# Kernel optimization log

Measured on AMD Instinct MI355X. Metric: run time of the kernel, lower is better.

Reference implementation:

```python
import jax, jax.numpy as jnp
import numpy as np

MAX_PIXELS = 8  # matches init max_pixels; width=256 matches input W


def _shift_one(img, cy, cx, vy, vx):
    # img: [C,H,W]; cy:[H] cx:[W] clamped source indices; vy/vx validity masks
    out = img[:, cy, :][:, :, cx]            # nearest gather == exact integer shift
    mask = (vy[:, None] & vx[None, :]).astype(img.dtype)  # zeros padding
    return out * mask


def setup_inputs() -> dict:
    key = jax.random.key(0)
    k1, k2 = jax.random.split(key)
    N, C, H, W = 128, 3, 256, 256
    inp = jax.random.normal(k1, (N, C, H, W), dtype=jnp.float32)
    # raw shifts in [0, 2*max_pixels]; reference subtracts MAX_PIXELS -> [-8, 8]
    shifts = jax.random.randint(k2, (N, 2), 0, 2 * MAX_PIXELS + 1, dtype=jnp.int32)
    return {"input": inp, "shifts": shifts}


def reference(input, shifts):
    # Equivalent of affine_grid(theta with bias=shift/(W/2)) + grid_sample(nearest,
    # padding_mode='zeros', align_corners=False): out[n,c,i,j] = in[n,c,i+dy,j+dx]
    # with zero padding out of range. shifts[:,0]=dx (x/width), shifts[:,1]=dy.
    N, C, H, W = input.shape
    s = shifts - MAX_PIXELS                       # [N,2] in [-max_pixels, max_pixels]
    j = jnp.arange(W, dtype=jnp.int32)
    i = jnp.arange(H, dtype=jnp.int32)
    src_x = j[None, :] + s[:, 0:1]                # [N,W]
    src_y = i[None, :] + s[:, 1:2]                # [N,H]
    vx = (src_x >= 0) & (src_x < W)
    vy = (src_y >= 0) & (src_y < H)
    cx = jnp.clip(src_x, 0, W - 1)
    cy = jnp.clip(src_y, 0, H - 1)
    return jax.vmap(_shift_one)(input, cy, cx, vy, vx)
```

## Files before the change

kernel.cpp:

```cpp
#include <hip/hip_runtime.h>


#define MAXPIX 8
#define W 256
#define H 256
#define CCH 3

__global__ __launch_bounds__(256) void shift_kernel(
    const float* __restrict__ in,
    const int* __restrict__ shifts,
    float* __restrict__ out,
    int total_rows)
{
    const int lane = threadIdx.x & 63;
    const int wave_in_block = threadIdx.x >> 6;
    const int rows_per_block = 256 / 64;
    int row = blockIdx.x * rows_per_block + wave_in_block;
    const int row_stride = gridDim.x * rows_per_block;

    for (; row < total_rows; row += row_stride) {
        const int i  = row & (H - 1);
        const int nc = row >> 8;
        const int n  = nc / CCH;

        const int sx = shifts[2 * n]     - MAXPIX;
        const int sy = shifts[2 * n + 1] - MAXPIX;

        const int src_y = i + sy;
        float4 v = {0.f, 0.f, 0.f, 0.f};
        if ((unsigned)src_y < (unsigned)H) {
            const float* __restrict__ src =
                in + ((long)nc * H + src_y) * W;
            const int j0 = (lane << 2) + sx;
            v.x = ((unsigned)(j0 + 0) < (unsigned)W) ? src[j0 + 0] : 0.f;
            v.y = ((unsigned)(j0 + 1) < (unsigned)W) ? src[j0 + 1] : 0.f;
            v.z = ((unsigned)(j0 + 2) < (unsigned)W) ? src[j0 + 2] : 0.f;
            v.w = ((unsigned)(j0 + 3) < (unsigned)W) ? src[j0 + 3] : 0.f;
        }
        *reinterpret_cast<float4*>(out + (long)row * W + (lane << 2)) = v;
    }
}

extern "C" void kernel_launch(void* const* d_in, const int* in_sizes, int n_in,
                              void* d_out, int out_size, void* d_ws, size_t ws_size,
                              hipStream_t stream) {
    const float* in     = (const float*)d_in[0];
    const int*   shifts = (const int*)d_in[1];
    float*       out    = (float*)d_out;

    const int total_rows = out_size / W;

    const int rows_per_block = 4;
    int blocks = (total_rows + rows_per_block - 1) / rows_per_block;
    if (blocks > 2048) blocks = 2048;

    shift_kernel<<<dim3(blocks), dim3(256), 0, stream>>>(in, shifts, out, total_rows);
}
```

Baseline: 38.19 us.

## Batch four rows per wave with branchless clamped loads and nontemporal stores

Replaces the grid-stride loop with a fixed mapping where each wave handles four consecutive rows. All loads are issued up front using clamped indices with masking afterwards, so there are no divergent branches and more memory requests are in flight. Output stores use nontemporal hints to avoid polluting cache, the shift index is made wave-uniform via readfirstlane, and the grid is no longer capped at 2048 blocks. The cost is more registers per thread and redundant loads for fully out-of-range rows.

```diff
diff --git a/kernel.cpp b/kernel.cpp
--- a/kernel.cpp
+++ b/kernel.cpp
@@ -6,6 +6,8 @@
 #define H 256
 #define CCH 3
 
+typedef float f32x4 __attribute__((ext_vector_type(4)));
+
 __global__ __launch_bounds__(256) void shift_kernel(
     const float* __restrict__ in,
     const int* __restrict__ shifts,
@@ -13,31 +15,51 @@
     int total_rows)
 {
     const int lane = threadIdx.x & 63;
-    const int wave_in_block = threadIdx.x >> 6;
-    const int rows_per_block = 256 / 64;
-    int row = blockIdx.x * rows_per_block + wave_in_block;
-    const int row_stride = gridDim.x * rows_per_block;
+    const int wid  = threadIdx.x >> 6;
+    constexpr int R = 4;
+    const int row0 = (blockIdx.x * 4 + wid) * R;
+    if (row0 >= total_rows) return;
 
-    for (; row < total_rows; row += row_stride) {
-        const int i  = row & (H - 1);
-        const int nc = row >> 8;
-        const int n  = nc / CCH;
+    f32x4 v[R];
+
+    #pragma unroll
+    for (int r = 0; r < R; ++r) {
+        int rr = row0 + r;
+        rr = min(rr, total_rows - 1);
+        const int i  = rr & (H - 1);
+        const int nc = rr >> 8;
+        int n = nc / CCH;
+        n = __builtin_amdgcn_readfirstlane(n);
 
         const int sx = shifts[2 * n]     - MAXPIX;
         const int sy = shifts[2 * n + 1] - MAXPIX;
 
-        const int src_y = i + sy;
-        float4 v = {0.f, 0.f, 0.f, 0.f};
-        if ((unsigned)src_y < (unsigned)H) {
-            const float* __restrict__ src =
-                in + ((long)nc * H + src_y) * W;
-            const int j0 = (lane << 2) + sx;
-            v.x = ((unsigned)(j0 + 0) < (unsigned)W) ? src[j0 + 0] : 0.f;
-            v.y = ((unsigned)(j0 + 1) < (unsigned)W) ? src[j0 + 1] : 0.f;
-            v.z = ((unsigned)(j0 + 2) < (unsigned)W) ? src[j0 + 2] : 0.f;
-            v.w = ((unsigned)(j0 + 3) < (unsigned)W) ? src[j0 + 3] : 0.f;
+        const int  syr = i + sy;
+        const int  syc = min(max(syr, 0), H - 1);
+        const bool vy  = (unsigned)syr < (unsigned)H;
+
+        const float* __restrict__ src = in + ((long)nc * H + syc) * W;
+        const int j0 = (lane << 2) + sx;
+
+        const int jc0 = min(max(j0 + 0, 0), W - 1);
+        const int jc1 = min(max(j0 + 1, 0), W - 1);
+        const int jc2 = min(max(j0 + 2, 0), W - 1);
+        const int jc3 = min(max(j0 + 3, 0), W - 1);
+        float x0 = src[jc0], x1 = src[jc1], x2 = src[jc2], x3 = src[jc3];
+
+        v[r].x = (vy && (unsigned)(j0 + 0) < (unsigned)W) ? x0 : 0.f;
+        v[r].y = (vy && (unsigned)(j0 + 1) < (unsigned)W) ? x1 : 0.f;
+        v[r].z = (vy && (unsigned)(j0 + 2) < (unsigned)W) ? x2 : 0.f;
+        v[r].w = (vy && (unsigned)(j0 + 3) < (unsigned)W) ? x3 : 0.f;
+    }
+
+    #pragma unroll
+    for (int r = 0; r < R; ++r) {
+        const int rr = row0 + r;
+        if (rr < total_rows) {
+            __builtin_nontemporal_store(v[r],
+                reinterpret_cast<f32x4*>(out + (long)rr * W + (lane << 2)));
         }
-        *reinterpret_cast<float4*>(out + (long)row * W + (lane << 2)) = v;
     }
 }
 
@@ -50,9 +72,8 @@
 
     const int total_rows = out_size / W;
 
-    const int rows_per_block = 4;
-    int blocks = (total_rows + rows_per_block - 1) / rows_per_block;
-    if (blocks > 2048) blocks = 2048;
+    const int rows_per_block = 16;
+    const int blocks = (total_rows + rows_per_block - 1) / rows_per_block;
 
     shift_kernel<<<dim3(blocks), dim3(256), 0, stream>>>(in, shifts, out, total_rows);
 }
```

Result: faster. 36.96 us (-3.2%).
